# Performance work log

Measured on AMD Instinct MI355X. Metric: run time of the kernel, lower is better.

The kernel has to match this reference:

```python
import jax, jax.numpy as jnp
import numpy as np
import math

B, S = 4, 1024
N_ITEMS, EMB = 50000, 128
H, D = 4, 32


def setup_inputs() -> dict:
    key = jax.random.key(0)
    ks = jax.random.split(key, 12)

    def lin(k, fan_in, fan_out):
        lim = 1.0 / math.sqrt(fan_in)
        return jax.random.uniform(k, (fan_in, fan_out), minval=-lim, maxval=lim, dtype=jnp.float32)

    inp = {}
    inp["sequence_item_indices"] = jax.random.randint(ks[0], (B, S), 0, N_ITEMS, dtype=jnp.int32)
    inp["sequence_correct_flags"] = jax.random.randint(ks[1], (B, S), 0, 2, dtype=jnp.int32)
    inp["sequence_time_gaps"] = jax.random.uniform(ks[2], (B, S), dtype=jnp.float32) * 100.0
    inp["item_emb"] = jax.random.normal(ks[3], (N_ITEMS, EMB), dtype=jnp.float32) * 0.02
    inp["ans_emb"] = jax.random.normal(ks[4], (2, EMB), dtype=jnp.float32) * 0.02
    inp["Wq"] = lin(ks[5], EMB, H * D); inp["bq"] = jnp.zeros((H * D,), jnp.float32)
    inp["Wk"] = lin(ks[6], EMB, H * D); inp["bk"] = jnp.zeros((H * D,), jnp.float32)
    inp["Wv"] = lin(ks[7], EMB, H * D); inp["bv"] = jnp.zeros((H * D,), jnp.float32)
    inp["Wh"] = lin(ks[8], 2 * EMB, EMB); inp["bh"] = jnp.zeros((EMB,), jnp.float32)
    inp["W1"] = lin(ks[9], H * D + EMB, EMB); inp["b1"] = jnp.zeros((EMB,), jnp.float32)
    inp["W2"] = lin(ks[10], EMB, 1); inp["b2"] = jnp.zeros((1,), jnp.float32)
    inp["theta_raw"] = jnp.zeros((H,), jnp.float32)
    return inp


def reference(sequence_item_indices, sequence_correct_flags, sequence_time_gaps,
              item_emb, ans_emb, Wq, bq, Wk, bk, Wv, bv, Wh, bh, W1, b1, W2, b2, theta_raw):
    Bb, Ss = sequence_item_indices.shape
    Hn = theta_raw.shape[0]
    Dd = Wq.shape[1] // Hn

    e = item_emb[sequence_item_indices]                      # [B,S,E]
    a = ans_emb[sequence_correct_flags]                      # [B,S,E]
    inter = jnp.concatenate([e, a], axis=-1) @ Wh + bh       # history_projection

    Q = (e @ Wq + bq).reshape(Bb, Ss, Hn, Dd)
    K = (e @ Wk + bk).reshape(Bb, Ss, Hn, Dd)
    V = (inter @ Wv + bv).reshape(Bb, Ss, Hn, Dd)
    scale = 1.0 / jnp.sqrt(jnp.float32(Dd))

    # self relevance per history position; per-target softmax over i<t done via exclusive prefix sums
    sr = jnp.sum(Q * K, axis=-1) * scale                     # [B,S,H]
    ex = jnp.exp(sr - jnp.max(sr, axis=1, keepdims=True))    # shift-invariant
    Ep = jnp.concatenate([jnp.zeros((Bb, 1, Hn), sr.dtype), jnp.cumsum(ex, axis=1)], axis=1)  # [B,S+1,H]

    g = jnp.maximum(sequence_time_gaps.astype(jnp.float32), 1.0)
    Pp = jnp.concatenate([jnp.zeros((Bb, 1), g.dtype), jnp.cumsum(g, axis=1)], axis=1)        # [B,S+1]

    t = jnp.arange(1, Ss)                                    # targets, T = S-1
    i = jnp.arange(Ss)                                       # history positions
    mask = i[None, :] < t[:, None]                           # [T,S]
    step = (t[:, None] - i[None, :]).astype(jnp.float32)     # arange(L,0,-1)[i] == t - i
    gap_diff = Pp[:, 1:Ss, None] - Pp[:, None, :Ss]          # [B,T,S]  sum_{j in [i,t)} clamp(gap,1)
    Et = Ep[:, 1:Ss, :]                                      # [B,T,H]  softmax normalizer Z_t
    rel = (Et[:, :, None, :] - Ep[:, None, :Ss, :]) / Et[:, :, None, :]  # cumulative relevance [B,T,S,H]
    pd = jnp.where(mask[None, :, :, None],
                   step[None, :, :, None] * gap_diff[..., None] * rel, 0.0)  # perceived distance

    theta = jax.nn.softplus(theta_raw) + 1e-4                # [H]
    decay = jnp.exp(-theta * pd)                             # [B,T,S,H]

    # candidate query at position t equals query_projection(item_embedding[t])
    raw = jnp.einsum('bthd,bihd->btih', Q[:, 1:], K) * scale # [B,T,S,H]
    scores = jnp.where(mask[None, :, :, None], raw * decay, -1e30)
    attn = jax.nn.softmax(scores, axis=2)                    # softmax over history positions
    ctx = jnp.einsum('btih,bihd->bthd', attn, V).reshape(Bb, Ss - 1, Hn * Dd)

    feat = jnp.concatenate([ctx, e[:, 1:]], axis=-1)
    h1 = jax.nn.relu(feat @ W1 + b1)                         # dropout is inference identity
    logit = (h1 @ W2 + b2)[..., 0]
    pred = jax.nn.sigmoid(logit)                             # [B,S-1]
    valid = jnp.ones((Bb, Ss - 1), dtype=bool)               # all positions valid (no padding)
    return pred, valid
```

## Files before the change

kernel.cpp:

```cpp
#include <hip/hip_runtime.h>
#include <math.h>

#define BSZ 4
#define SSZ 1024
#define EMBD 128
#define HN 4
#define DN 32
#define TQ (SSZ - 1)
#define NROWS (BSZ * TQ)

typedef __attribute__((ext_vector_type(8))) short bf16x8;
typedef __attribute__((ext_vector_type(4))) short bf16x4;
typedef __attribute__((ext_vector_type(4))) float f32x4;

static __device__ __forceinline__ unsigned short f2bf(float x) {
    union { float f; unsigned u; } v; v.f = x;
    unsigned r = v.u + 0x7fffu + ((v.u >> 16) & 1u);
    return (unsigned short)(r >> 16);
}
static __device__ __forceinline__ bf16x8 cvt8(const float4 a, const float4 b) {
    bf16x8 v;
    v[0] = (short)f2bf(a.x); v[1] = (short)f2bf(a.y);
    v[2] = (short)f2bf(a.z); v[3] = (short)f2bf(a.w);
    v[4] = (short)f2bf(b.x); v[5] = (short)f2bf(b.y);
    v[6] = (short)f2bf(b.z); v[7] = (short)f2bf(b.w);
    return v;
}

__global__ __launch_bounds__(256)
void embed4_kernel(const int* __restrict__ idx, const int* __restrict__ flg,
                   const float* __restrict__ item_emb, const float* __restrict__ ans_emb,
                   const float* __restrict__ Wq, const float* __restrict__ bq,
                   const float* __restrict__ Wk, const float* __restrict__ bk,
                   const float* __restrict__ Wv, const float* __restrict__ bv,
                   const float* __restrict__ Wh, const float* __restrict__ bh_bias,
                   unsigned short* __restrict__ Qts, unsigned short* __restrict__ Kts,
                   unsigned short* __restrict__ Vts,
                   float* __restrict__ ec, float* __restrict__ srw)
{
    __shared__ __align__(16) unsigned short esb[16][136];
    __shared__ __align__(16) unsigned short asb[16][136];
    __shared__ __align__(16) unsigned short intb[16][136];
    __shared__ __align__(16) unsigned short Wt[128][40];

    const int tid = threadIdx.x;
    const int tok0 = blockIdx.x * 16;
    const int b = blockIdx.x >> 6;
    const int s0 = tok0 & 1023;
    const int w = tid >> 6, lane = tid & 63;
    const int quad = lane >> 4, col = lane & 15;

    {
        const int tk = tid >> 4;
        const int d0 = (tid & 15) * 8;
        const int tok = tok0 + tk;
        const float* esrc = item_emb + (size_t)idx[tok] * EMBD + d0;
        const float* asrc = ans_emb + (size_t)flg[tok] * EMBD + d0;
        const float4 e0 = *(const float4*)esrc;
        const float4 e1 = *(const float4*)(esrc + 4);
        const float4 a0 = *(const float4*)asrc;
        const float4 a1 = *(const float4*)(asrc + 4);
        *(float4*)(ec + (size_t)tok * EMBD + d0) = e0;
        *(float4*)(ec + (size_t)tok * EMBD + d0 + 4) = e1;
        *(bf16x8*)&esb[tk][d0] = cvt8(e0, e1);
        *(bf16x8*)&asb[tk][d0] = cvt8(a0, a1);
    }

    const int jb = (tid & 31) * 4;
    const int ib = (tid >> 5) * 4;
    float rr[4][4];

    #define WSRC(R) ((R) < 8 ? Wh + (size_t)(R) * 4096                     \
                  : (R) < 12 ? Wq + (size_t)((R) - 8) * 4096               \
                  : (R) < 16 ? Wk + (size_t)((R) - 12) * 4096              \
                  : Wv + (size_t)((R) - 16) * 4096)
    #define LOADW(P)                                                       \
    {                                                                      \
        const float* _p = (P);                                             \
        *(float4*)rr[0] = *(const float4*)(_p + (ib + 0) * 128 + jb);      \
        *(float4*)rr[1] = *(const float4*)(_p + (ib + 1) * 128 + jb);      \
        *(float4*)rr[2] = *(const float4*)(_p + (ib + 2) * 128 + jb);      \
        *(float4*)rr[3] = *(const float4*)(_p + (ib + 3) * 128 + jb);      \
    }
    #define STOREW                                                         \
    {                                                                      \
        _Pragma("unroll")                                                  \
        for (int jj = 0; jj < 4; jj++) {                                   \
            bf16x4 v;                                                      \
            v[0] = (short)f2bf(rr[0][jj]); v[1] = (short)f2bf(rr[1][jj]);  \
            v[2] = (short)f2bf(rr[2][jj]); v[3] = (short)f2bf(rr[3][jj]);  \
            *(bf16x4*)&Wt[jb + jj][ib] = v;                                \
        }                                                                  \
    }

    f32x4 accI[2] = {{0.f,0.f,0.f,0.f},{0.f,0.f,0.f,0.f}};
    f32x4 accQ[2] = {{0.f,0.f,0.f,0.f},{0.f,0.f,0.f,0.f}};
    f32x4 accK[2] = {{0.f,0.f,0.f,0.f},{0.f,0.f,0.f,0.f}};
    f32x4 accV[2] = {{0.f,0.f,0.f,0.f},{0.f,0.f,0.f,0.f}};

    LOADW(WSRC(0));
    #pragma unroll
    for (int r = 0; r < 20; r++) {
        __syncthreads();
        STOREW;
        __syncthreads();
        if (r < 19) LOADW(WSRC(r + 1));

        const unsigned short (*Ab)[136] = (r < 4) ? esb : (r < 8) ? asb
                                        : (r < 16) ? esb : intb;
        const int koff = ((r < 8) ? (r & 3) : (r < 12) ? (r - 8)
                        : (r < 16) ? (r - 12) : (r - 16)) * 32;
        const bf16x8 af = *(const bf16x8*)&Ab[col][koff + quad * 8];
        f32x4* acc = (r < 8) ? accI : (r < 12) ? accQ : (r < 16) ? accK : accV;
        #pragma unroll
        for (int ntl = 0; ntl < 2; ntl++) {
            const bf16x8 bf = *(const bf16x8*)&Wt[w * 32 + ntl * 16 + col][quad * 8];
            acc[ntl] = __builtin_amdgcn_mfma_f32_16x16x32_bf16(af, bf, acc[ntl], 0, 0, 0);
        }
        if (r == 7) {
            #pragma unroll
            for (int ntl = 0; ntl < 2; ntl++) {
                const int j = w * 32 + ntl * 16 + col;
                const float bb = bh_bias[j];
                #pragma unroll
                for (int r4 = 0; r4 < 4; r4++)
                    intb[quad * 4 + r4][j] = f2bf(accI[ntl][r4] + bb);
            }
        }
    }
    #undef LOADW
    #undef STOREW
    #undef WSRC

    const int bhn = b * HN + w;
    const float scale = 0.17677669529663687f;
    float p[4] = {0.f, 0.f, 0.f, 0.f};
    #pragma unroll
    for (int ntl = 0; ntl < 2; ntl++) {
        const int j = w * 32 + ntl * 16 + col;
        const float bQ = bq[j], bK = bk[j], bV = bv[j];
        #pragma unroll
        for (int r = 0; r < 4; r++) {
            const float qv = accQ[ntl][r] + bQ;
            const float kv = accK[ntl][r] + bK;
            const int s = s0 + quad * 4 + r;
            const size_t o = ((size_t)bhn * SSZ + s) * DN + ntl * 16 + col;
            Qts[o] = f2bf(qv * scale);
            Kts[o] = f2bf(kv);
            Vts[o] = f2bf(accV[ntl][r] + bV);
            p[r] = fmaf(qv, kv, p[r]);
        }
    }
    #pragma unroll
    for (int r = 0; r < 4; r++) {
        float pr = p[r];
        pr += __shfl_xor(pr, 1, 64);
        pr += __shfl_xor(pr, 2, 64);
        pr += __shfl_xor(pr, 4, 64);
        pr += __shfl_xor(pr, 8, 64);
        if (col == 0)
            srw[(size_t)bhn * SSZ + s0 + quad * 4 + r] = pr * scale;
    }
}

__global__ __launch_bounds__(256)
void attn4_kernel(const unsigned short* __restrict__ Qts,
                  const unsigned short* __restrict__ Kts,
                  const unsigned short* __restrict__ Vts,
                  const float* __restrict__ srw, const float* __restrict__ gaps,
                  const float* __restrict__ theta_raw, float* __restrict__ csw,
                  float* __restrict__ ls)
{
    __shared__ __align__(16) unsigned short Ks[64][40];
    __shared__ __align__(16) unsigned short Vs[32][72];
    __shared__ __align__(16) unsigned short Ps[4][16][72];
    __shared__ float EpS[SSZ + 1];
    __shared__ float PpS[SSZ + 1];
    __shared__ float wtot[4];

    const int bid = blockIdx.x;
    const int half = bid & 1;
    const int qt = (bid >> 1) & 15;
    const int bh = bid >> 5;
    const int b = bh >> 2, h = bh & 3;
    const int tid = threadIdx.x;
    const int w = tid >> 6, lane = tid & 63;
    const int quad = lane >> 4, col = lane & 15;
    const int t0 = qt * 64 + 1;

    const int nc = qt + 1;
    const int c0r = half ? (nc >> 1) : 0;
    const int c1r = half ? nc : (nc >> 1);

    {
        const float4 sv = *(const float4*)(srw + (size_t)bh * SSZ + tid * 4);
        const float e0 = __expf(sv.x);
        const float p0 = e0;
        const float p1 = p0 + __expf(sv.y);
        const float p2 = p1 + __expf(sv.z);
        const float p3 = p2 + __expf(sv.w);
        float s = p3;
        #pragma unroll
        for (int d = 1; d < 64; d <<= 1) {
            const float t = __shfl_up(s, d, 64);
            if (lane >= d) s += t;
        }
        if (lane == 63) wtot[w] = s;
        __syncthreads();
        float base = s - p3;
        for (int ww = 0; ww < w; ww++) base += wtot[ww];
        EpS[tid * 4 + 1] = base + p0;
        EpS[tid * 4 + 2] = base + p1;
        EpS[tid * 4 + 3] = base + p2;
        EpS[tid * 4 + 4] = base + p3;
        if (tid == 0) EpS[0] = 0.0f;
    }
    {
        const float4 gv = *(const float4*)(gaps + (size_t)b * SSZ + tid * 4);
        const float p0 = fmaxf(gv.x, 1.0f);
        const float p1 = p0 + fmaxf(gv.y, 1.0f);
        const float p2 = p1 + fmaxf(gv.z, 1.0f);
        const float p3 = p2 + fmaxf(gv.w, 1.0f);
        float s = p3;
        #pragma unroll
        for (int d = 1; d < 64; d <<= 1) {
            const float t = __shfl_up(s, d, 64);
            if (lane >= d) s += t;
        }
        __syncthreads();
        if (lane == 63) wtot[w] = s;
        __syncthreads();
        float base = s - p3;
        for (int ww = 0; ww < w; ww++) base += wtot[ww];
        PpS[tid * 4 + 1] = base + p0;
        PpS[tid * 4 + 2] = base + p1;
        PpS[tid * 4 + 3] = base + p2;
        PpS[tid * 4 + 4] = base + p3;
        if (tid == 0) PpS[0] = 0.0f;
    }
    __syncthreads();

    const float theta = logf(1.0f + __expf(theta_raw[h])) + 1e-4f;
    const float nth = -theta;
    float Ept[4], Ppt[4], iEp[4], tft[4];
    int qrow[4], tq[4];
    #pragma unroll
    for (int r = 0; r < 4; r++) {
        qrow[r] = w * 16 + quad * 4 + r;
        tq[r] = t0 + qrow[r];
        tft[r] = (float)tq[r];
        Ept[r] = EpS[tq[r]];
        Ppt[r] = PpS[tq[r]];
        iEp[r] = 1.0f / Ept[r];
    }

    bf16x8 aq;
    {
        int t = t0 + w * 16 + col; if (t > 1023) t = 1023;
        aq = *(const bf16x8*)(Qts + ((size_t)(bh * SSZ + t)) * DN + quad * 8);
    }

    f32x4 acc0 = {0.f, 0.f, 0.f, 0.f};
    f32x4 acc1 = {0.f, 0.f, 0.f, 0.f};
    float lsum[4] = {0.f, 0.f, 0.f, 0.f};

    const int i_st = tid >> 2;
    const int d0 = (tid & 3) * 8;
    bf16x8 kreg = *(const bf16x8*)(Kts + ((size_t)(bh * SSZ + c0r * 64 + i_st)) * DN + d0);
    bf16x8 vreg = *(const bf16x8*)(Vts + ((size_t)(bh * SSZ + c0r * 64 + i_st)) * DN + d0);

    for (int c = c0r; c < c1r; c++) {
        __syncthreads();
        *(bf16x8*)&Ks[i_st][d0] = kreg;
        #pragma unroll
        for (int k2 = 0; k2 < 8; k2++) Vs[d0 + k2][i_st] = (unsigned short)vreg[k2];
        __syncthreads();
        if (c + 1 < c1r) {
            const size_t o = ((size_t)(bh * SSZ + (c + 1) * 64 + i_st)) * DN + d0;
            kreg = *(const bf16x8*)(Kts + o);
            vreg = *(const bf16x8*)(Vts + o);
        }

        const bool full = (c < qt);
        #pragma unroll
        for (int nt = 0; nt < 4; nt++) {
            const bf16x8 bk = *(const bf16x8*)&Ks[nt * 16 + col][quad * 8];
            f32x4 z = {0.f, 0.f, 0.f, 0.f};
            f32x4 raw = __builtin_amdgcn_mfma_f32_16x16x32_bf16(aq, bk, z, 0, 0, 0);
            const int il = nt * 16 + col;
            const int i_ = c * 64 + il;
            const float Epi = EpS[i_];
            const float Ppi = PpS[i_];
            const float fi = (float)i_;
            #pragma unroll
            for (int r = 0; r < 4; r++) {
                const float pdv = (tft[r] - fi) * (Ppt[r] - Ppi) * ((Ept[r] - Epi) * iEp[r]);
                const float sc  = raw[r] * __expf(nth * pdv);
                float p = __expf(sc);
                p = (full || il <= qrow[r]) ? p : 0.0f;
                lsum[r] += p;
                Ps[w][quad * 4 + r][il] = f2bf(p);
            }
        }
        #pragma unroll
        for (int ks = 0; ks < 2; ks++) {
            const bf16x8 ap = *(const bf16x8*)&Ps[w][col][ks * 32 + quad * 8];
            const bf16x8 bv0 = *(const bf16x8*)&Vs[col][ks * 32 + quad * 8];
            const bf16x8 bv1 = *(const bf16x8*)&Vs[16 + col][ks * 32 + quad * 8];
            acc0 = __builtin_amdgcn_mfma_f32_16x16x32_bf16(ap, bv0, acc0, 0, 0, 0);
            acc1 = __builtin_amdgcn_mfma_f32_16x16x32_bf16(ap, bv1, acc1, 0, 0, 0);
        }
    }

    #pragma unroll
    for (int r = 0; r < 4; r++) {
        float lr = lsum[r];
        #pragma unroll
        for (int msk = 8; msk >= 1; msk >>= 1) lr += __shfl_xor(lr, msk, 64);
        lsum[r] = lr;
    }
    const size_t cswh = (size_t)half * NROWS * EMBD;
    const size_t lsh  = (size_t)half * (HN * BSZ * SSZ) + ((size_t)bh << 10);
    #pragma unroll
    for (int r = 0; r < 4; r++) {
        if (tq[r] <= 1023) {
            float* dst = csw + cswh + ((size_t)(b * TQ + (tq[r] - 1))) * EMBD + h * DN;
            dst[col]      = acc0[r];
            dst[16 + col] = acc1[r];
            if (col == 0) ls[lsh + tq[r]] = lsum[r];
        }
    }
}

__global__ __launch_bounds__(256)
void mlp3_kernel(const float* __restrict__ csw, const float* __restrict__ ls,
                 const float* __restrict__ ec,
                 const float* __restrict__ W1, const float* __restrict__ b1,
                 const float* __restrict__ W2, const float* __restrict__ b2,
                 float* __restrict__ out)
{
    __shared__ __align__(16) unsigned short featb[32][264];
    __shared__ __align__(16) unsigned short W1t[128][264];
    __shared__ float sred[4][16];

    const int tid = threadIdx.x;
    const int r0 = blockIdx.x * 32;
    const int w = tid >> 6, lane = tid & 63;
    const int quad = lane >> 4, col = lane & 15;
    const int mt = w & 1, nh = w >> 1;

    {
        const int jb = (tid & 31) * 4;
        const int ib = (tid >> 5) * 4;
        for (int ic = 0; ic < 8; ic++) {
            const int i0 = ic * 32 + ib;
            float rr[4][4];
            *(float4*)rr[0] = *(const float4*)(W1 + (size_t)(i0 + 0) * 128 + jb);
            *(float4*)rr[1] = *(const float4*)(W1 + (size_t)(i0 + 1) * 128 + jb);
            *(float4*)rr[2] = *(const float4*)(W1 + (size_t)(i0 + 2) * 128 + jb);
            *(float4*)rr[3] = *(const float4*)(W1 + (size_t)(i0 + 3) * 128 + jb);
            #pragma unroll
            for (int jj = 0; jj < 4; jj++) {
                bf16x4 v;
                v[0] = (short)f2bf(rr[0][jj]); v[1] = (short)f2bf(rr[1][jj]);
                v[2] = (short)f2bf(rr[2][jj]); v[3] = (short)f2bf(rr[3][jj]);
                *(bf16x4*)&W1t[jb + jj][i0] = v;
            }
        }
    }
    {
        const int rr = tid >> 3;
        const int c0 = (tid & 7) * 32;
        int row = r0 + rr; if (row >= NROWS) row = NROWS - 1;
        if (c0 < 128) {
            const int bb = row / TQ;
            const int tt = row - bb * TQ + 1;
            const int hh = c0 >> 5;
            const size_t lsi = ((size_t)(bb * HN + hh) << 10) + tt;
            const float l0 = ls[lsi];
            const float l1 = ls[(size_t)(HN * BSZ * SSZ) + lsi];
            const float inv = 1.0f / (l0 + l1);
            const float* s0 = csw + (size_t)row * EMBD + c0;
            const float* s1 = csw + (size_t)NROWS * EMBD + (size_t)row * EMBD + c0;
            #pragma unroll
            for (int g = 0; g < 4; g++) {
                float4 f0 = ((const float4*)s0)[g * 2];
                float4 f1 = ((const float4*)s0)[g * 2 + 1];
                const float4 g0 = ((const float4*)s1)[g * 2];
                const float4 g1 = ((const float4*)s1)[g * 2 + 1];
                f0.x = (f0.x + g0.x) * inv; f0.y = (f0.y + g0.y) * inv;
                f0.z = (f0.z + g0.z) * inv; f0.w = (f0.w + g0.w) * inv;
                f1.x = (f1.x + g1.x) * inv; f1.y = (f1.y + g1.y) * inv;
                f1.z = (f1.z + g1.z) * inv; f1.w = (f1.w + g1.w) * inv;
                *(bf16x8*)&featb[rr][c0 + g * 8] = cvt8(f0, f1);
            }
        } else {
            const int bb = row / TQ;
            const int tt = row - bb * TQ + 1;
            const float* src = ec + ((size_t)(bb * SSZ + tt)) * EMBD + (c0 - 128);
            #pragma unroll
            for (int g = 0; g < 4; g++) {
                const float4 f0 = ((const float4*)src)[g * 2];
                const float4 f1 = ((const float4*)src)[g * 2 + 1];
                *(bf16x8*)&featb[rr][c0 + g * 8] = cvt8(f0, f1);
            }
        }
    }
    __syncthreads();

    float s[4] = {0.f, 0.f, 0.f, 0.f};
    #pragma unroll
    for (int ntl = 0; ntl < 4; ntl++) {
        const int nt = nh * 4 + ntl;
        f32x4 acc = {0.f, 0.f, 0.f, 0.f};
        #pragma unroll
        for (int kc = 0; kc < 8; kc++) {
            const bf16x8 af = *(const bf16x8*)&featb[mt * 16 + col][kc * 32 + quad * 8];
            const bf16x8 bf = *(const bf16x8*)&W1t[nt * 16 + col][kc * 32 + quad * 8];
            acc = __builtin_amdgcn_mfma_f32_16x16x32_bf16(af, bf, acc, 0, 0, 0);
        }
        const int j = nt * 16 + col;
        const float b1j = b1[j], w2j = W2[j];
        #pragma unroll
        for (int r = 0; r < 4; r++)
            s[r] = fmaf(fmaxf(acc[r] + b1j, 0.0f), w2j, s[r]);
    }
    #pragma unroll
    for (int r = 0; r < 4; r++) {
        float sr = s[r];
        sr += __shfl_xor(sr, 1, 64);
        sr += __shfl_xor(sr, 2, 64);
        sr += __shfl_xor(sr, 4, 64);
        sr += __shfl_xor(sr, 8, 64);
        if (col == 0) sred[w][quad * 4 + r] = sr;
    }
    __syncthreads();
    if (tid < 32) {
        const int mt2 = tid >> 4, rr = tid & 15;
        const float logit = sred[mt2][rr] + sred[mt2 + 2][rr] + b2[0];
        const int grow = r0 + tid;
        if (grow < NROWS) {
            out[grow] = 1.0f / (1.0f + __expf(-logit));
            out[NROWS + grow] = 1.0f;
        }
    }
}

extern "C" void kernel_launch(void* const* d_in, const int* in_sizes, int n_in,
                              void* d_out, int out_size, void* d_ws, size_t ws_size,
                              hipStream_t stream)
{
    const int*   idx       = (const int*)d_in[0];
    const int*   flg       = (const int*)d_in[1];
    const float* gaps      = (const float*)d_in[2];
    const float* item_emb  = (const float*)d_in[3];
    const float* ans_emb   = (const float*)d_in[4];
    const float* Wq        = (const float*)d_in[5];
    const float* bq        = (const float*)d_in[6];
    const float* Wk        = (const float*)d_in[7];
    const float* bk        = (const float*)d_in[8];
    const float* Wv        = (const float*)d_in[9];
    const float* bv        = (const float*)d_in[10];
    const float* Wh        = (const float*)d_in[11];
    const float* bh        = (const float*)d_in[12];
    const float* W1        = (const float*)d_in[13];
    const float* b1        = (const float*)d_in[14];
    const float* W2        = (const float*)d_in[15];
    const float* b2        = (const float*)d_in[16];
    const float* theta_raw = (const float*)d_in[17];
    (void)in_sizes; (void)n_in; (void)ws_size;

    const size_t QKV = (size_t)BSZ * HN * SSZ * DN;
    unsigned short* Qts = (unsigned short*)d_ws;
    unsigned short* Kts = Qts + QKV;
    unsigned short* Vts = Kts + QKV;
    float* ec  = (float*)(Vts + QKV);
    float* srw = ec + (size_t)BSZ * SSZ * EMBD;
    float* csw = srw + (size_t)BSZ * HN * SSZ;
    float* ls  = csw + 2 * (size_t)NROWS * EMBD;

    float* out = (float*)d_out;

    embed4_kernel<<<BSZ * SSZ / 16, 256, 0, stream>>>(
        idx, flg, item_emb, ans_emb, Wq, bq, Wk, bk, Wv, bv, Wh, bh,
        Qts, Kts, Vts, ec, srw);
    attn4_kernel<<<BSZ * HN * 32, 256, 0, stream>>>(
        Qts, Kts, Vts, srw, gaps, theta_raw, csw, ls);
    mlp3_kernel<<<(NROWS + 31) / 32, 256, 0, stream>>>(
        csw, ls, ec, W1, b1, W2, b2, out);
}
```

Measured before the change: 145.3 us.

## Fuse three kernels into one cooperative kernel with grid syncs

Merges the embed, attention and MLP kernels into a single cooperative launch of 512 blocks, separated by grid-wide barriers and sharing a union of LDS layouts. The goal is to remove two kernel launch gaps and the tail-drain between stages. The MLP stage now stages W1 in two 128-row halves so its LDS footprint fits the union, at the cost of an extra block barrier and the grid sync overhead. If the cooperative launch fails, the code falls back to the original three launches.

Result: slower. 275.3 us (+89.6%).

```diff
diff --git a/kernel.cpp b/kernel.cpp
--- a/kernel.cpp
+++ b/kernel.cpp
@@ -1,4 +1,5 @@
 #include <hip/hip_runtime.h>
+#include <hip/hip_cooperative_groups.h>
 #include <math.h>
 
 #define BSZ 4
@@ -27,21 +28,36 @@
     return v;
 }
 
-__global__ __launch_bounds__(256)
-void embed4_kernel(const int* __restrict__ idx, const int* __restrict__ flg,
-                   const float* __restrict__ item_emb, const float* __restrict__ ans_emb,
-                   const float* __restrict__ Wq, const float* __restrict__ bq,
-                   const float* __restrict__ Wk, const float* __restrict__ bk,
-                   const float* __restrict__ Wv, const float* __restrict__ bv,
-                   const float* __restrict__ Wh, const float* __restrict__ bh_bias,
-                   unsigned short* __restrict__ Qts, unsigned short* __restrict__ Kts,
-                   unsigned short* __restrict__ Vts,
-                   float* __restrict__ ec, float* __restrict__ srw)
-{
-    __shared__ __align__(16) unsigned short esb[16][136];
-    __shared__ __align__(16) unsigned short asb[16][136];
-    __shared__ __align__(16) unsigned short intb[16][136];
-    __shared__ __align__(16) unsigned short Wt[128][40];
+struct __align__(16) SMemA {
+    unsigned short esb[16][136], asb[16][136], intb[16][136];
+    unsigned short Wt[128][40];
+};
+struct __align__(16) SMemB {
+    unsigned short Ks[64][40], Vs[32][72], Ps[4][16][72];
+    float EpS[SSZ + 1], PpS[SSZ + 1], wtot[4];
+};
+struct __align__(16) SMemC {
+    unsigned short featb[32][264];
+    unsigned short W1t[128][136];
+    float sred[4][16];
+};
+union __align__(16) SMemU { SMemA a; SMemB b; SMemC c; };
+
+__device__ __forceinline__ void phaseA_body(SMemA& am,
+    const int* __restrict__ idx, const int* __restrict__ flg,
+    const float* __restrict__ item_emb, const float* __restrict__ ans_emb,
+    const float* __restrict__ Wq, const float* __restrict__ bq,
+    const float* __restrict__ Wk, const float* __restrict__ bk,
+    const float* __restrict__ Wv, const float* __restrict__ bv,
+    const float* __restrict__ Wh, const float* __restrict__ bh_bias,
+    unsigned short* __restrict__ Qts, unsigned short* __restrict__ Kts,
+    unsigned short* __restrict__ Vts,
+    float* __restrict__ ec, float* __restrict__ srw)
+{
+    unsigned short (&esb)[16][136] = am.esb;
+    unsigned short (&asb)[16][136] = am.asb;
+    unsigned short (&intb)[16][136] = am.intb;
+    unsigned short (&Wt)[128][40] = am.Wt;
 
     const int tid = threadIdx.x;
     const int tok0 = blockIdx.x * 16;
@@ -163,20 +179,19 @@
     }
 }
 
-__global__ __launch_bounds__(256)
-void attn4_kernel(const unsigned short* __restrict__ Qts,
-                  const unsigned short* __restrict__ Kts,
-                  const unsigned short* __restrict__ Vts,
-                  const float* __restrict__ srw, const float* __restrict__ gaps,
-                  const float* __restrict__ theta_raw, float* __restrict__ csw,
-                  float* __restrict__ ls)
-{
-    __shared__ __align__(16) unsigned short Ks[64][40];
-    __shared__ __align__(16) unsigned short Vs[32][72];
-    __shared__ __align__(16) unsigned short Ps[4][16][72];
-    __shared__ float EpS[SSZ + 1];
-    __shared__ float PpS[SSZ + 1];
-    __shared__ float wtot[4];
+__device__ __forceinline__ void phaseB_body(SMemB& bm,
+    const unsigned short* __restrict__ Qts, const unsigned short* __restrict__ Kts,
+    const unsigned short* __restrict__ Vts,
+    const float* __restrict__ srw, const float* __restrict__ gaps,
+    const float* __restrict__ theta_raw, float* __restrict__ csw,
+    float* __restrict__ ls)
+{
+    unsigned short (&Ks)[64][40] = bm.Ks;
+    unsigned short (&Vs)[32][72] = bm.Vs;
+    unsigned short (&Ps)[4][16][72] = bm.Ps;
+    float (&EpS)[SSZ + 1] = bm.EpS;
+    float (&PpS)[SSZ + 1] = bm.PpS;
+    float (&wtot)[4] = bm.wtot;
 
     const int bid = blockIdx.x;
     const int half = bid & 1;
@@ -332,42 +347,25 @@
     }
 }
 
-__global__ __launch_bounds__(256)
-void mlp3_kernel(const float* __restrict__ csw, const float* __restrict__ ls,
-                 const float* __restrict__ ec,
-                 const float* __restrict__ W1, const float* __restrict__ b1,
-                 const float* __restrict__ W2, const float* __restrict__ b2,
-                 float* __restrict__ out)
-{
-    __shared__ __align__(16) unsigned short featb[32][264];
-    __shared__ __align__(16) unsigned short W1t[128][264];
-    __shared__ float sred[4][16];
+__device__ __forceinline__ void phaseC_body(SMemC& cm,
+    const float* __restrict__ csw, const float* __restrict__ ls,
+    const float* __restrict__ ec,
+    const float* __restrict__ W1, const float* __restrict__ b1,
+    const float* __restrict__ W2, const float* __restrict__ b2,
+    float* __restrict__ out)
+{
+    unsigned short (&featb)[32][264] = cm.featb;
+    unsigned short (&W1t)[128][136] = cm.W1t;
+    float (&sred)[4][16] = cm.sred;
 
     const int tid = threadIdx.x;
     const int r0 = blockIdx.x * 32;
     const int w = tid >> 6, lane = tid & 63;
     const int quad = lane >> 4, col = lane & 15;
     const int mt = w & 1, nh = w >> 1;
-
-    {
-        const int jb = (tid & 31) * 4;
-        const int ib = (tid >> 5) * 4;
-        for (int ic = 0; ic < 8; ic++) {
-            const int i0 = ic * 32 + ib;
-            float rr[4][4];
-            *(float4*)rr[0] = *(const float4*)(W1 + (size_t)(i0 + 0) * 128 + jb);
-            *(float4*)rr[1] = *(const float4*)(W1 + (size_t)(i0 + 1) * 128 + jb);
-            *(float4*)rr[2] = *(const float4*)(W1 + (size_t)(i0 + 2) * 128 + jb);
-            *(float4*)rr[3] = *(const float4*)(W1 + (size_t)(i0 + 3) * 128 + jb);
-            #pragma unroll
-            for (int jj = 0; jj < 4; jj++) {
-                bf16x4 v;
-                v[0] = (short)f2bf(rr[0][jj]); v[1] = (short)f2bf(rr[1][jj]);
-                v[2] = (short)f2bf(rr[2][jj]); v[3] = (short)f2bf(rr[3][jj]);
-                *(bf16x4*)&W1t[jb + jj][i0] = v;
-            }
-        }
-    }
+    const int jb = (tid & 31) * 4;
+    const int ib = (tid >> 5) * 4;
+
     {
         const int rr = tid >> 3;
         const int c0 = (tid & 7) * 32;
@@ -406,24 +404,50 @@
             }
         }
     }
-    __syncthreads();
+
+    f32x4 acc[4] = {{0.f,0.f,0.f,0.f},{0.f,0.f,0.f,0.f},
+                    {0.f,0.f,0.f,0.f},{0.f,0.f,0.f,0.f}};
+    #pragma unroll
+    for (int p = 0; p < 2; p++) {
+        if (p) __syncthreads();
+        #pragma unroll
+        for (int ic = 0; ic < 4; ic++) {
+            const int i0 = ic * 32 + ib;
+            const int gi = p * 128 + i0;
+            float rr4[4][4];
+            *(float4*)rr4[0] = *(const float4*)(W1 + (size_t)(gi + 0) * 128 + jb);
+            *(float4*)rr4[1] = *(const float4*)(W1 + (size_t)(gi + 1) * 128 + jb);
+            *(float4*)rr4[2] = *(const float4*)(W1 + (size_t)(gi + 2) * 128 + jb);
+            *(float4*)rr4[3] = *(const float4*)(W1 + (size_t)(gi + 3) * 128 + jb);
+            #pragma unroll
+            for (int jj = 0; jj < 4; jj++) {
+                bf16x4 v;
+                v[0] = (short)f2bf(rr4[0][jj]); v[1] = (short)f2bf(rr4[1][jj]);
+                v[2] = (short)f2bf(rr4[2][jj]); v[3] = (short)f2bf(rr4[3][jj]);
+                *(bf16x4*)&W1t[jb + jj][i0] = v;
+            }
+        }
+        __syncthreads();
+        #pragma unroll
+        for (int ntl = 0; ntl < 4; ntl++) {
+            const int nt = nh * 4 + ntl;
+            #pragma unroll
+            for (int kc = 0; kc < 4; kc++) {
+                const bf16x8 af = *(const bf16x8*)&featb[mt * 16 + col][p * 128 + kc * 32 + quad * 8];
+                const bf16x8 bf = *(const bf16x8*)&W1t[nt * 16 + col][kc * 32 + quad * 8];
+                acc[ntl] = __builtin_amdgcn_mfma_f32_16x16x32_bf16(af, bf, acc[ntl], 0, 0, 0);
+            }
+        }
+    }
 
     float s[4] = {0.f, 0.f, 0.f, 0.f};
     #pragma unroll
     for (int ntl = 0; ntl < 4; ntl++) {
-        const int nt = nh * 4 + ntl;
-        f32x4 acc = {0.f, 0.f, 0.f, 0.f};
-        #pragma unroll
-        for (int kc = 0; kc < 8; kc++) {
-            const bf16x8 af = *(const bf16x8*)&featb[mt * 16 + col][kc * 32 + quad * 8];
-            const bf16x8 bf = *(const bf16x8*)&W1t[nt * 16 + col][kc * 32 + quad * 8];
-            acc = __builtin_amdgcn_mfma_f32_16x16x32_bf16(af, bf, acc, 0, 0, 0);
-        }
-        const int j = nt * 16 + col;
+        const int j = (nh * 4 + ntl) * 16 + col;
         const float b1j = b1[j], w2j = W2[j];
         #pragma unroll
         for (int r = 0; r < 4; r++)
-            s[r] = fmaf(fmaxf(acc[r] + b1j, 0.0f), w2j, s[r]);
+            s[r] = fmaf(fmaxf(acc[ntl][r] + b1j, 0.0f), w2j, s[r]);
     }
     #pragma unroll
     for (int r = 0; r < 4; r++) {
@@ -444,6 +468,68 @@
             out[NROWS + grow] = 1.0f;
         }
     }
+}
+
+__global__ __launch_bounds__(256)
+void embed4_kernel(const int* __restrict__ idx, const int* __restrict__ flg,
+                   const float* __restrict__ item_emb, const float* __restrict__ ans_emb,
+                   const float* __restrict__ Wq, const float* __restrict__ bq,
+                   const float* __restrict__ Wk, const float* __restrict__ bk,
+                   const float* __restrict__ Wv, const float* __restrict__ bv,
+                   const float* __restrict__ Wh, const float* __restrict__ bh_bias,
+                   unsigned short* __restrict__ Qts, unsigned short* __restrict__ Kts,
+                   unsigned short* __restrict__ Vts,
+                   float* __restrict__ ec, float* __restrict__ srw)
+{
+    __shared__ __align__(16) SMemA sm;
+    phaseA_body(sm, idx, flg, item_emb, ans_emb, Wq, bq, Wk, bk, Wv, bv,
+                Wh, bh_bias, Qts, Kts, Vts, ec, srw);
+}
+
+__global__ __launch_bounds__(256)
+void attn4_kernel(const unsigned short* __restrict__ Qts,
+                  const unsigned short* __restrict__ Kts,
+                  const unsigned short* __restrict__ Vts,
+                  const float* __restrict__ srw, const float* __restrict__ gaps,
+                  const float* __restrict__ theta_raw, float* __restrict__ csw,
+                  float* __restrict__ ls)
+{
+    __shared__ __align__(16) SMemB sm;
+    phaseB_body(sm, Qts, Kts, Vts, srw, gaps, theta_raw, csw, ls);
+}
+
+__global__ __launch_bounds__(256)
+void mlp3_kernel(const float* __restrict__ csw, const float* __restrict__ ls,
+                 const float* __restrict__ ec,
+                 const float* __restrict__ W1, const float* __restrict__ b1,
+                 const float* __restrict__ W2, const float* __restrict__ b2,
+                 float* __restrict__ out)
+{
+    __shared__ __align__(16) SMemC sm;
+    phaseC_body(sm, csw, ls, ec, W1, b1, W2, b2, out);
+}
+
+__global__ __launch_bounds__(256, 2)
+void fused_kernel(const int* idx, const int* flg, const float* gaps,
+                  const float* item_emb, const float* ans_emb,
+                  const float* Wq, const float* bq, const float* Wk, const float* bk,
+                  const float* Wv, const float* bv, const float* Wh, const float* bh_bias,
+                  const float* W1, const float* b1, const float* W2, const float* b2,
+                  const float* theta_raw,
+                  unsigned short* Qts, unsigned short* Kts, unsigned short* Vts,
+                  float* ec, float* srw, float* csw, float* ls, float* out)
+{
+    __shared__ __align__(16) SMemU sm;
+    cooperative_groups::grid_group grid = cooperative_groups::this_grid();
+
+    if (blockIdx.x < 256)
+        phaseA_body(sm.a, idx, flg, item_emb, ans_emb, Wq, bq, Wk, bk, Wv, bv,
+                    Wh, bh_bias, Qts, Kts, Vts, ec, srw);
+    grid.sync();
+    phaseB_body(sm.b, Qts, Kts, Vts, srw, gaps, theta_raw, csw, ls);
+    grid.sync();
+    if (blockIdx.x < 128)
+        phaseC_body(sm.c, csw, ls, ec, W1, b1, W2, b2, out);
 }
 
 extern "C" void kernel_launch(void* const* d_in, const int* in_sizes, int n_in,
@@ -481,11 +567,23 @@
 
     float* out = (float*)d_out;
 
-    embed4_kernel<<<BSZ * SSZ / 16, 256, 0, stream>>>(
-        idx, flg, item_emb, ans_emb, Wq, bq, Wk, bk, Wv, bv, Wh, bh,
-        Qts, Kts, Vts, ec, srw);
-    attn4_kernel<<<BSZ * HN * 32, 256, 0, stream>>>(
-        Qts, Kts, Vts, srw, gaps, theta_raw, csw, ls);
-    mlp3_kernel<<<(NROWS + 31) / 32, 256, 0, stream>>>(
-        csw, ls, ec, W1, b1, W2, b2, out);
-}
+    void* args[] = {
+        (void*)&idx, (void*)&flg, (void*)&gaps, (void*)&item_emb, (void*)&ans_emb,
+        (void*)&Wq, (void*)&bq, (void*)&Wk, (void*)&bk, (void*)&Wv, (void*)&bv,
+        (void*)&Wh, (void*)&bh, (void*)&W1, (void*)&b1, (void*)&W2, (void*)&b2,
+        (void*)&theta_raw,
+        (void*)&Qts, (void*)&Kts, (void*)&Vts, (void*)&ec, (void*)&srw,
+        (void*)&csw, (void*)&ls, (void*)&out
+    };
+    const hipError_t cerr = hipLaunchCooperativeKernel(
+        (void*)fused_kernel, dim3(512), dim3(256), args, 0, stream);
+    if (cerr != hipSuccess) {
+        embed4_kernel<<<BSZ * SSZ / 16, 256, 0, stream>>>(
+            idx, flg, item_emb, ans_emb, Wq, bq, Wk, bk, Wv, bv, Wh, bh,
+            Qts, Kts, Vts, ec, srw);
+        attn4_kernel<<<BSZ * HN * 32, 256, 0, stream>>>(
+            Qts, Kts, Vts, srw, gaps, theta_raw, csw, ls);
+        mlp3_kernel<<<(NROWS + 31) / 32, 256, 0, stream>>>(
+            csw, ls, ec, W1, b1, W2, b2, out);
+    }
+}
```
